# Kernel optimization log

Hardware: AMD Instinct MI355X
Metric: run time of the kernel (lower is better)

The kernel has to match this reference:

```python
import jax, jax.numpy as jnp
import numpy as np

N_EMBED = 2048
N_HEAD = 16
N_GROUP = 4
D_HEAD = N_EMBED // N_HEAD  # 128
GROUP_SIZE = N_HEAD // N_GROUP  # 4
SLIDING_WINDOW = 512
ATTENTION_SINK = 4
POS = 0
ROPE_BASE = 10000.0


def _rope(x, pos):
    # x: (B, T, H, d) -> rotate-half RoPE applied along last dim
    B, T, H, d = x.shape
    half = d // 2
    inv_freq = 1.0 / (ROPE_BASE ** (jnp.arange(half, dtype=jnp.float32) * 2.0 / d))
    t = jnp.arange(T, dtype=jnp.float32) + pos
    ang = t[:, None] * inv_freq[None, :]           # (T, half)
    cos = jnp.cos(ang)[None, :, None, :].astype(x.dtype)
    sin = jnp.sin(ang)[None, :, None, :].astype(x.dtype)
    x1, x2 = x[..., :half], x[..., half:]
    return jnp.concatenate([x1 * cos - x2 * sin, x1 * sin + x2 * cos], axis=-1)


def _sliding_mask(q_len, kv_len):
    i = jnp.arange(q_len)[:, None]
    j = jnp.arange(kv_len)[None, :]
    causal = i >= j
    sink = j < ATTENTION_SINK
    local = j >= i - SLIDING_WINDOW
    return causal & (local | sink)  # (q_len, kv_len) bool


def setup_inputs() -> dict:
    key = jax.random.key(0)
    ks = jax.random.split(key, 9)
    s_in = 1.0 / np.sqrt(N_EMBED)
    x = jax.random.normal(ks[0], (2, 2048, N_EMBED), dtype=jnp.float32)
    # Linear weights stored as (in, out): y = x @ W + b
    Wq = jax.random.uniform(ks[1], (N_EMBED, N_HEAD * D_HEAD), jnp.float32, -s_in, s_in)
    bq = jax.random.uniform(ks[2], (N_HEAD * D_HEAD,), jnp.float32, -s_in, s_in)
    Wk = jax.random.uniform(ks[3], (N_EMBED, N_GROUP * D_HEAD), jnp.float32, -s_in, s_in)
    bk = jax.random.uniform(ks[4], (N_GROUP * D_HEAD,), jnp.float32, -s_in, s_in)
    Wv = jax.random.uniform(ks[5], (N_EMBED, N_GROUP * D_HEAD), jnp.float32, -s_in, s_in)
    bv = jax.random.uniform(ks[6], (N_GROUP * D_HEAD,), jnp.float32, -s_in, s_in)
    Wo = jax.random.uniform(ks[7], (N_EMBED, N_EMBED), jnp.float32, -s_in, s_in)
    bo = jax.random.uniform(ks[8], (N_EMBED,), jnp.float32, -s_in, s_in)
    return {"x": x, "Wq": Wq, "bq": bq, "Wk": Wk, "bk": bk,
            "Wv": Wv, "bv": bv, "Wo": Wo, "bo": bo}


def reference(x, Wq, bq, Wk, bk, Wv, bv, Wo, bo):
    B, T, C = x.shape
    scale = D_HEAD ** -0.5
    Q = (x @ Wq + bq).reshape(B, T, N_HEAD, D_HEAD)
    K = (x @ Wk + bk).reshape(B, T, N_GROUP, D_HEAD)
    V = (x @ Wv + bv).reshape(B, T, N_GROUP, D_HEAD)
    Q = _rope(Q, POS)
    K = _rope(K, POS)
    # (B, G, group, T, d) -- native GQA broadcast instead of repeat_interleave
    Q = Q.transpose(0, 2, 1, 3).reshape(B, N_GROUP, GROUP_SIZE, T, D_HEAD)
    K = K.transpose(0, 2, 1, 3)  # (B, G, T, d)
    V = V.transpose(0, 2, 1, 3)
    scores = jnp.einsum('bghtd,bgsd->bghts', Q, K) * scale  # (B,G,h,T,S)
    mask = _sliding_mask(T, T)[None, None, None, :, :]
    neg = jnp.finfo(scores.dtype).min
    scores = jnp.where(mask, scores, neg)
    W = jax.nn.softmax(scores, axis=-1)
    out = jnp.einsum('bghts,bgsd->bghtd', W, V)  # (B,G,h,T,d)
    out = out.reshape(B, N_HEAD, T, D_HEAD).transpose(0, 2, 1, 3).reshape(B, T, C)
    return out @ Wo + bo
```

## Files before the change

### kernel.cpp

```cpp
#include <hip/hip_runtime.h>
#include <hip/hip_bf16.h>
#include <cstdint>
#include <cstddef>


typedef short s16;
typedef short short8 __attribute__((ext_vector_type(8)));
typedef short s16x4  __attribute__((ext_vector_type(4)));
typedef float f32x4  __attribute__((ext_vector_type(4)));

#define MFMA16(a, b, c) __builtin_amdgcn_mfma_f32_16x16x32_bf16((a), (b), (c), 0, 0, 0)

__device__ __forceinline__ float bf2f(s16 u) {
    union { float f; uint32_t i; } v;
    v.i = ((uint32_t)(uint16_t)u) << 16;
    return v.f;
}
__device__ __forceinline__ s16 f2bf(float f) {
    union { float f; uint32_t i; } v;
    v.f = f;
    uint32_t r = v.i + 0x7FFFu + ((v.i >> 16) & 1u);
    return (s16)(r >> 16);
}

__device__ __forceinline__ void gload16(const s16* g, s16* l) {
    __builtin_amdgcn_global_load_lds(
        (const __attribute__((address_space(1))) void*)g,
        (__attribute__((address_space(3))) void*)l, 16, 0, 0);
}

__global__ __launch_bounds__(256)
void cast_bf16(const float* __restrict__ in, s16* __restrict__ out)
{
    size_t i = ((size_t)blockIdx.x * 256 + threadIdx.x) * 8;
    f32x4 f0 = *(const f32x4*)(in + i);
    f32x4 f1 = *(const f32x4*)(in + i + 4);
    short8 h;
    h[0]=f2bf(f0[0]); h[1]=f2bf(f0[1]); h[2]=f2bf(f0[2]); h[3]=f2bf(f0[3]);
    h[4]=f2bf(f1[0]); h[5]=f2bf(f1[1]); h[6]=f2bf(f1[2]); h[7]=f2bf(f1[3]);
    *(short8*)(out + i) = h;
}

__global__ __launch_bounds__(256)
void castT3(const float* __restrict__ Wq, const float* __restrict__ Wk,
            const float* __restrict__ Wv, s16* __restrict__ out)
{
    int z = blockIdx.z;
    const float* in; s16* dst; int N;
    if (z == 0)      { in = Wq; dst = out;                        N = 2048; }
    else if (z == 1) { in = Wk; dst = out + (size_t)2048 * 2048;  N = 512; }
    else             { in = Wv; dst = out + (size_t)2560 * 2048;  N = 512; }
    int n0 = blockIdx.x * 32, k0 = blockIdx.y * 32;
    if (n0 >= N) return;

    __shared__ float t[32][33];
    int tx = threadIdx.x & 31, ty = threadIdx.x >> 5;
    for (int i = 0; i < 32; i += 8)
        t[ty + i][tx] = in[(size_t)(k0 + ty + i) * N + n0 + tx];
    __syncthreads();
    for (int i = 0; i < 32; i += 8)
        dst[(size_t)(n0 + ty + i) * 2048 + k0 + tx] = f2bf(t[tx][ty + i]);
}

__global__ __launch_bounds__(256)
void castT(const float* __restrict__ in, s16* __restrict__ out)
{
    __shared__ float t[32][33];
    int n0 = blockIdx.x * 32, k0 = blockIdx.y * 32;
    int tx = threadIdx.x & 31, ty = threadIdx.x >> 5;
    for (int i = 0; i < 32; i += 8)
        t[ty + i][tx] = in[(size_t)(k0 + ty + i) * 2048 + n0 + tx];
    __syncthreads();
    for (int i = 0; i < 32; i += 8)
        out[(size_t)(n0 + ty + i) * 2048 + k0 + tx] = f2bf(t[tx][ty + i]);
}

template <int MODE>
__global__ __launch_bounds__(256)
void gemm_lds(const s16* __restrict__ A, const s16* __restrict__ Bt,
              const float* __restrict__ b0, const float* __restrict__ b1,
              const float* __restrict__ b2,
              void* __restrict__ o0, void* __restrict__ o1, void* __restrict__ o2,
              int M, int N, int K)
{
    __shared__ s16 As[128 * 32];
    __shared__ s16 Bs[128 * 32];

    const int tid  = threadIdx.x;
    const int m0   = blockIdx.x * 128, n0 = blockIdx.y * 128;
    const int lane = tid & 63, wv = tid >> 6;
    const int wm   = (wv >> 1) * 64, wn = (wv & 1) * 64;
    const int fr   = lane & 15, fq = lane >> 4;

    const int srow = wv * 16 + (lane >> 2);
    const int koff = (lane & 3) * 8;
    const s16* ga0 = A  + (size_t)(m0 + srow) * K + koff;
    const s16* ga1 = A  + (size_t)(m0 + 64 + srow) * K + koff;
    const s16* gb0 = Bt + (size_t)(n0 + srow) * K + koff;
    const s16* gb1 = Bt + (size_t)(n0 + 64 + srow) * K + koff;
    s16* la0 = &As[(wv * 16) * 32];
    s16* la1 = &As[(64 + wv * 16) * 32];
    s16* lb0 = &Bs[(wv * 16) * 32];
    s16* lb1 = &Bs[(64 + wv * 16) * 32];

    const s16* pa[4];
    const s16* pb[4];
    #pragma unroll
    for (int i = 0; i < 4; i++) {
        pa[i] = &As[(wm + i * 16 + fr) * 32 + fq * 8];
        pb[i] = &Bs[(wn + i * 16 + fr) * 32 + fq * 8];
    }

    f32x4 acc[4][4] = {};

    for (int k0 = 0; k0 < K; k0 += 32) {
        __syncthreads();
        gload16(ga0 + k0, la0);
        gload16(ga1 + k0, la1);
        gload16(gb0 + k0, lb0);
        gload16(gb1 + k0, lb1);
        __syncthreads();

        short8 af[4], bfr[4];
        #pragma unroll
        for (int i = 0; i < 4; i++) af[i] = *(const short8*)pa[i];
        #pragma unroll
        for (int i = 0; i < 4; i++) bfr[i] = *(const short8*)pb[i];

        #pragma unroll
        for (int mi = 0; mi < 4; mi++)
            #pragma unroll
            for (int ni = 0; ni < 4; ni++)
                acc[mi][ni] = MFMA16(af[mi], bfr[ni], acc[mi][ni]);
    }

    #pragma unroll
    for (int mi = 0; mi < 4; mi++)
        #pragma unroll
        for (int ni = 0; ni < 4; ni++)
            #pragma unroll
            for (int r = 0; r < 4; r++) {
                int m = m0 + wm + mi * 16 + fq * 4 + r;
                int n = n0 + wn + ni * 16 + fr;
                float v = acc[mi][ni][r];
                if (MODE == 0) {
                    if (n < 2048)
                        ((s16*)o0)[(size_t)m * 2048 + n] = f2bf(v + b0[n]);
                    else if (n < 2560)
                        ((s16*)o1)[(size_t)m * 512 + (n - 2048)] = f2bf(v + b1[n - 2048]);
                    else
                        ((s16*)o2)[(size_t)(n - 2560) * 4096 + m] = f2bf(v + b2[n - 2560]);
                } else {
                    ((float*)o0)[(size_t)m * N + n] = v + b0[n];
                }
            }
}

__global__ __launch_bounds__(256)
void rope2_kernel(s16* __restrict__ Qb, s16* __restrict__ Kb)
{
    int bx = blockIdx.x;
    s16* buf; int nheads; int idx;
    if (bx < 16384) { buf = Qb; nheads = 16; idx = bx * 256 + threadIdx.x; }
    else            { buf = Kb; nheads = 4;  idx = (bx - 16384) * 256 + threadIdx.x; }

    int i   = idx & 63;
    int hi  = idx >> 6;
    int h   = hi % nheads;
    int row = hi / nheads;
    int t   = row & 2047;

    float inv_freq = __powf(10000.0f, -(float)i * (1.0f / 64.0f));
    float ang = (float)t * inv_freq;
    float c = cosf(ang);
    float s = sinf(ang);

    size_t base = (size_t)row * ((size_t)nheads * 128) + (size_t)h * 128 + i;
    float x1 = bf2f(buf[base]);
    float x2 = bf2f(buf[base + 64]);
    buf[base]      = f2bf(x1 * c - x2 * s);
    buf[base + 64] = f2bf(x1 * s + x2 * c);
}

__global__ __launch_bounds__(256)
void attn_kernel(const s16* __restrict__ Q, const s16* __restrict__ Kb,
                 const s16* __restrict__ Vt, s16* __restrict__ At)
{
    __shared__ s16 Ks[2][32][136];
    __shared__ s16 Vs[2][128][40];
    __shared__ s16 Ps[4][16][40];

    const int b = blockIdx.z;
    const int h = blockIdx.y, g = h >> 2;
    const int t0 = (31 - blockIdx.x) * 64;
    const int tid = threadIdx.x, lane = tid & 63, wv = tid >> 6;
    const int fr = lane & 15, fq = lane >> 4;
    const int tw = t0 + wv * 16;
    s16* O = At + (size_t)b * 4194304;

    const float SCL2 = 0.12751743f;
    const float NEG  = -1e9f;
    const float THR2 = 11.541560f;

    int kr[2], kc[2], vd[2], vc[2];
    const s16 *gK[2], *gV[2];
    #pragma unroll
    for (int it = 0; it < 2; it++) {
        int idx = it * 2048 + tid * 8;
        kr[it] = idx >> 7;  kc[it] = idx & 127;
        vd[it] = idx >> 5;  vc[it] = idx & 31;
        gK[it] = Kb + (size_t)(b * 2048 + kr[it]) * 512 + g * 128 + kc[it];
        gV[it] = Vt + (size_t)(g * 128 + vd[it]) * 4096 + b * 2048 + vc[it];
    }

    short8 qf[4];
    {
        const s16* qrow = Q + (size_t)(b * 2048 + tw + fr) * 2048 + h * 128 + fq * 8;
        qf[0] = *(const short8*)(qrow);
        qf[1] = *(const short8*)(qrow + 32);
        qf[2] = *(const short8*)(qrow + 64);
        qf[3] = *(const short8*)(qrow + 96);
    }

    f32x4 Oacc[8] = {};
    float m2 = NEG, l_s = 0.0f;
    const int tq = tw + fr;

    int lo = t0 - 512; if (lo < 0) lo = 0;
    const int c0   = lo >> 5;
    const int cend = (t0 + 63) >> 5;
    const int nch  = cend - c0 + 1 + (c0 > 0 ? 1 : 0);

    #define CHUNKBASE(ic) ((((c0) > 0) ? ((ic) == 0 ? 0 : c0 + (ic) - 1) : (ic)) * 32)

    short8 kpre[2], vpre[2];
    {
        int kb = CHUNKBASE(0);
        #pragma unroll
        for (int it = 0; it < 2; it++) {
            kpre[it] = *(const short8*)(gK[it] + (size_t)kb * 512);
            vpre[it] = *(const short8*)(gV[it] + kb);
        }
        #pragma unroll
        for (int it = 0; it < 2; it++) {
            *(short8*)&Ks[0][kr[it]][kc[it]] = kpre[it];
            *(short8*)&Vs[0][vd[it]][vc[it]] = vpre[it];
        }
    }
    __syncthreads();

    for (int ic = 0; ic < nch; ic++) {
        const int cur = ic & 1;
        const int kbase = CHUNKBASE(ic);
        const bool pre = (ic + 1 < nch);
        if (pre) {
            int kb = CHUNKBASE(ic + 1);
            #pragma unroll
            for (int it = 0; it < 2; it++) {
                kpre[it] = *(const short8*)(gK[it] + (size_t)kb * 512);
                vpre[it] = *(const short8*)(gV[it] + kb);
            }
        }

        f32x4 sc[2] = {{0.f,0.f,0.f,0.f},{0.f,0.f,0.f,0.f}};
        __builtin_amdgcn_s_setprio(1);
        #pragma unroll
        for (int kn = 0; kn < 2; kn++)
            #pragma unroll
            for (int dc = 0; dc < 4; dc++) {
                short8 kf = *(const short8*)&Ks[cur][kn * 16 + fr][dc * 32 + fq * 8];
                sc[kn] = MFMA16(kf, qf[dc], sc[kn]);
            }
        __builtin_amdgcn_s_setprio(0);

        float sv[8];
        #pragma unroll
        for (int kn = 0; kn < 2; kn++)
            #pragma unroll
            for (int r = 0; r < 4; r++) {
                int j = kbase + kn * 16 + fq * 4 + r;
                bool ok = (j <= tq) && ((j >= tq - 512) || (j < 4));
                sv[kn * 4 + r] = ok ? sc[kn][r] * SCL2 : NEG;
            }

        float cm = fmaxf(sv[0], sv[1]);
        #pragma unroll
        for (int i = 2; i < 8; i++) cm = fmaxf(cm, sv[i]);
        cm = fmaxf(cm, __shfl_xor(cm, 16));
        cm = fmaxf(cm, __shfl_xor(cm, 32));

        if (__any(cm > m2 + THR2)) {
            float nm    = fmaxf(m2, cm);
            float alpha = exp2f(m2 - nm);
            m2  = nm;
            l_s *= alpha;
            #pragma unroll
            for (int r = 0; r < 4; r++) {
                float ar = __shfl(alpha, (lane & 48) + fq * 4 + r);
                #pragma unroll
                for (int n0 = 0; n0 < 8; n0++) Oacc[n0][r] *= ar;
            }
        }

        float p[8], ps = 0.0f;
        #pragma unroll
        for (int i = 0; i < 8; i++) { p[i] = exp2f(sv[i] - m2); ps += p[i]; }
        ps += __shfl_xor(ps, 16);
        ps += __shfl_xor(ps, 32);
        l_s += ps;

        s16x4 w0, w1;
        #pragma unroll
        for (int r = 0; r < 4; r++) { w0[r] = f2bf(p[r]); w1[r] = f2bf(p[4 + r]); }
        *(s16x4*)&Ps[wv][fr][fq * 4]      = w0;
        *(s16x4*)&Ps[wv][fr][16 + fq * 4] = w1;
        __threadfence_block();
        short8 pf = *(const short8*)&Ps[wv][fr][fq * 8];

        __builtin_amdgcn_s_setprio(1);
        #pragma unroll
        for (int n0 = 0; n0 < 8; n0++) {
            short8 vf = *(const short8*)&Vs[cur][n0 * 16 + fr][fq * 8];
            Oacc[n0] = MFMA16(pf, vf, Oacc[n0]);
        }
        __builtin_amdgcn_s_setprio(0);

        if (pre) {
            #pragma unroll
            for (int it = 0; it < 2; it++) {
                *(short8*)&Ks[cur ^ 1][kr[it]][kc[it]] = kpre[it];
                *(short8*)&Vs[cur ^ 1][vd[it]][vc[it]] = vpre[it];
            }
            __syncthreads();
        }
    }

    float linv[4];
    #pragma unroll
    for (int r = 0; r < 4; r++)
        linv[r] = 1.0f / __shfl(l_s, (lane & 48) + fq * 4 + r);
    #pragma unroll
    for (int n0 = 0; n0 < 8; n0++)
        #pragma unroll
        for (int r = 0; r < 4; r++) {
            int t = tw + fq * 4 + r;
            O[(size_t)t * 2048 + h * 128 + n0 * 16 + fr] =
                f2bf(Oacc[n0][r] * linv[r]);
        }
}

extern "C" void kernel_launch(void* const* d_in, const int* in_sizes, int n_in,
                              void* d_out, int out_size, void* d_ws, size_t ws_size,
                              hipStream_t stream)
{
    const float* x  = (const float*)d_in[0];
    const float* Wq = (const float*)d_in[1];
    const float* bq = (const float*)d_in[2];
    const float* Wk = (const float*)d_in[3];
    const float* bk = (const float*)d_in[4];
    const float* Wv = (const float*)d_in[5];
    const float* bv = (const float*)d_in[6];
    const float* Wo = (const float*)d_in[7];
    const float* bo = (const float*)d_in[8];
    float* out = (float*)d_out;

    if (ws_size < 33554432) return;

    char* ws = (char*)d_ws;
    s16* xb    = (s16*)(ws + 0);
    s16* At    = (s16*)(ws + 0);
    s16* Wqkvt = (s16*)(ws + 16777216);
    s16* Wot   = (s16*)(ws + 16777216);
    s16* Qb    = (s16*)d_out;
    s16* Kb    = (s16*)((char*)d_out + 16777216);
    s16* Vt    = (s16*)((char*)d_out + 20971520);

    cast_bf16<<<4096, 256, 0, stream>>>(x, xb);

    castT3<<<dim3(64, 64, 3), 256, 0, stream>>>(Wq, Wk, Wv, Wqkvt);

    gemm_lds<0><<<dim3(32, 24), 256, 0, stream>>>(xb, Wqkvt, bq, bk, bv,
                                                  Qb, Kb, Vt, 4096, 3072, 2048);

    rope2_kernel<<<20480, 256, 0, stream>>>(Qb, Kb);

    castT<<<dim3(64, 64), 256, 0, stream>>>(Wo, Wot);

    attn_kernel<<<dim3(32, 16, 2), 256, 0, stream>>>(Qb, Kb, Vt, At);

    gemm_lds<2><<<dim3(32, 16), 256, 0, stream>>>(At, Wot, bo, nullptr, nullptr,
                                                  out, nullptr, nullptr,
                                                  4096, 2048, 2048);
}
```

Before: 347.1 us.

## Replace 128x128 GEMM with double-buffered swizzled 256x256 tile GEMM

Both projection GEMMs now use a 256x256 block tile with 8 waves, K-step 64, XOR-swizzled LDS layout, and double-buffered shared memory. Global loads for the next K tile are issued in quarters interleaved with the MFMA phases, with explicit waitcnt/barrier scheduling and setprio. This aims to raise arithmetic intensity, cut LDS bank conflicts and hide global latency. Grids shrink to 192 and 128 blocks, which may underfill the 256 CUs, and 128 KB of LDS per block limits occupancy.

Result: slower. 493.3 us (+42.1%).

```diff
diff --git a/kernel.cpp b/kernel.cpp
--- a/kernel.cpp
+++ b/kernel.cpp
@@ -76,66 +76,109 @@
 }
 
 template <int MODE>
-__global__ __launch_bounds__(256)
-void gemm_lds(const s16* __restrict__ A, const s16* __restrict__ Bt,
-              const float* __restrict__ b0, const float* __restrict__ b1,
-              const float* __restrict__ b2,
-              void* __restrict__ o0, void* __restrict__ o1, void* __restrict__ o2,
-              int M, int N, int K)
-{
-    __shared__ s16 As[128 * 32];
-    __shared__ s16 Bs[128 * 32];
+__global__ __launch_bounds__(512, 2)
+void gemm256(const s16* __restrict__ A, const s16* __restrict__ Bt,
+             const float* __restrict__ b0, const float* __restrict__ b1,
+             const float* __restrict__ b2,
+             void* __restrict__ o0, void* __restrict__ o1, void* __restrict__ o2,
+             int M, int N, int K)
+{
+    __shared__ s16 As[2][16384];
+    __shared__ s16 Bs[2][16384];
 
     const int tid  = threadIdx.x;
-    const int m0   = blockIdx.x * 128, n0 = blockIdx.y * 128;
     const int lane = tid & 63, wv = tid >> 6;
-    const int wm   = (wv >> 1) * 64, wn = (wv & 1) * 64;
-    const int fr   = lane & 15, fq = lane >> 4;
-
-    const int srow = wv * 16 + (lane >> 2);
-    const int koff = (lane & 3) * 8;
-    const s16* ga0 = A  + (size_t)(m0 + srow) * K + koff;
-    const s16* ga1 = A  + (size_t)(m0 + 64 + srow) * K + koff;
-    const s16* gb0 = Bt + (size_t)(n0 + srow) * K + koff;
-    const s16* gb1 = Bt + (size_t)(n0 + 64 + srow) * K + koff;
-    s16* la0 = &As[(wv * 16) * 32];
-    s16* la1 = &As[(64 + wv * 16) * 32];
-    s16* lb0 = &Bs[(wv * 16) * 32];
-    s16* lb1 = &Bs[(64 + wv * 16) * 32];
-
-    const s16* pa[4];
-    const s16* pb[4];
-    #pragma unroll
-    for (int i = 0; i < 4; i++) {
-        pa[i] = &As[(wm + i * 16 + fr) * 32 + fq * 8];
-        pb[i] = &Bs[(wn + i * 16 + fr) * 32 + fq * 8];
-    }
-
-    f32x4 acc[4][4] = {};
-
-    for (int k0 = 0; k0 < K; k0 += 32) {
-        __syncthreads();
-        gload16(ga0 + k0, la0);
-        gload16(ga1 + k0, la1);
-        gload16(gb0 + k0, lb0);
-        gload16(gb1 + k0, lb1);
-        __syncthreads();
-
-        short8 af[4], bfr[4];
-        #pragma unroll
-        for (int i = 0; i < 4; i++) af[i] = *(const short8*)pa[i];
-        #pragma unroll
-        for (int i = 0; i < 4; i++) bfr[i] = *(const short8*)pb[i];
-
-        #pragma unroll
-        for (int mi = 0; mi < 4; mi++)
-            #pragma unroll
-            for (int ni = 0; ni < 4; ni++)
-                acc[mi][ni] = MFMA16(af[mi], bfr[ni], acc[mi][ni]);
-    }
-
-    #pragma unroll
-    for (int mi = 0; mi < 4; mi++)
+    const int m0 = blockIdx.x * 256, n0 = blockIdx.y * 256;
+    const int wm = (wv >> 2) * 128;
+    const int wn = (wv & 3) * 64;
+    const int fr = lane & 15, fq = lane >> 4;
+    const int hA = wm >> 7;
+    const int hB = wn >> 7;
+    const int NT = K >> 6;
+
+    const int rs = wv * 8 + (lane >> 3);
+    const int cg = ((lane & 7) ^ (rs & 7)) << 3;
+    const s16* gs[2][2][2];
+    #pragma unroll
+    for (int hh = 0; hh < 2; hh++) {
+        gs[0][hh][0] = A  + (size_t)(m0 + hh * 128 + rs)      * K + cg;
+        gs[0][hh][1] = A  + (size_t)(m0 + hh * 128 + rs + 64) * K + cg;
+        gs[1][hh][0] = Bt + (size_t)(n0 + hh * 128 + rs)      * K + cg;
+        gs[1][hh][1] = Bt + (size_t)(n0 + hh * 128 + rs + 64) * K + cg;
+    }
+
+    const int kx0 = (fq ^ (fr & 7)) << 4;
+    const int kx1 = kx0 ^ 64;
+    const char* aBase[2] = {
+        (const char*)&As[0][0] + hA * 16384 + fr * 128,
+        (const char*)&As[1][0] + hA * 16384 + fr * 128 };
+    const char* bBase[2] = {
+        (const char*)&Bs[0][0] + hB * 16384 + ((wn & 64) + fr) * 128,
+        (const char*)&Bs[1][0] + hB * 16384 + ((wn & 64) + fr) * 128 };
+
+    f32x4 acc[8][4] = {};
+
+    #pragma unroll
+    for (int u = 0; u < 4; u++) {
+        const int op = u >> 1, hh = u & 1;
+        s16* d = (op ? &Bs[0][0] : &As[0][0]) + hh * 8192 + wv * 512;
+        gload16(gs[op][hh][0], d);
+        gload16(gs[op][hh][1], d + 4096);
+    }
+    asm volatile("s_waitcnt vmcnt(0)");
+    __builtin_amdgcn_sched_barrier(0);
+    __builtin_amdgcn_s_barrier();
+
+    short8 bf[4][2];
+    for (int t = 0; t < NT; t++) {
+        const int rb = t & 1, wb = rb ^ 1;
+        const bool pre = (t + 1 < NT);
+        #pragma unroll
+        for (int q = 0; q < 4; q++) {
+            short8 af[2][2];
+            #pragma unroll
+            for (int m2 = 0; m2 < 2; m2++)
+                #pragma unroll
+                for (int k2 = 0; k2 < 2; k2++)
+                    af[m2][k2] = *(const short8*)(aBase[rb] + (2 * q + m2) * 2048
+                                                  + (k2 ? kx1 : kx0));
+            if (q == 0) {
+                #pragma unroll
+                for (int ni = 0; ni < 4; ni++)
+                    #pragma unroll
+                    for (int k2 = 0; k2 < 2; k2++)
+                        bf[ni][k2] = *(const short8*)(bBase[rb] + ni * 2048
+                                                      + (k2 ? kx1 : kx0));
+            }
+            if (pre) {
+                const int op = q >> 1, hh = q & 1;
+                s16* d = (op ? &Bs[wb][0] : &As[wb][0]) + hh * 8192 + wv * 512;
+                gload16(gs[op][hh][0] + (t + 1) * 64, d);
+                gload16(gs[op][hh][1] + (t + 1) * 64, d + 4096);
+            }
+            __builtin_amdgcn_s_barrier();
+            asm volatile("s_waitcnt lgkmcnt(0)");
+            __builtin_amdgcn_sched_barrier(0);
+            __builtin_amdgcn_s_setprio(1);
+            #pragma unroll
+            for (int m2 = 0; m2 < 2; m2++)
+                #pragma unroll
+                for (int ni = 0; ni < 4; ni++)
+                    #pragma unroll
+                    for (int k2 = 0; k2 < 2; k2++)
+                        acc[2 * q + m2][ni] =
+                            MFMA16(af[m2][k2], bf[ni][k2], acc[2 * q + m2][ni]);
+            __builtin_amdgcn_s_setprio(0);
+            if (q == 3) {
+                asm volatile("s_waitcnt vmcnt(0)");
+                __builtin_amdgcn_sched_barrier(0);
+            }
+            __builtin_amdgcn_s_barrier();
+        }
+    }
+
+    #pragma unroll
+    for (int mi = 0; mi < 8; mi++)
         #pragma unroll
         for (int ni = 0; ni < 4; ni++)
             #pragma unroll
@@ -379,8 +422,8 @@
 
     castT3<<<dim3(64, 64, 3), 256, 0, stream>>>(Wq, Wk, Wv, Wqkvt);
 
-    gemm_lds<0><<<dim3(32, 24), 256, 0, stream>>>(xb, Wqkvt, bq, bk, bv,
-                                                  Qb, Kb, Vt, 4096, 3072, 2048);
+    gemm256<0><<<dim3(16, 12), 512, 0, stream>>>(xb, Wqkvt, bq, bk, bv,
+                                                 Qb, Kb, Vt, 4096, 3072, 2048);
 
     rope2_kernel<<<20480, 256, 0, stream>>>(Qb, Kb);
 
@@ -388,7 +431,7 @@
 
     attn_kernel<<<dim3(32, 16, 2), 256, 0, stream>>>(Qb, Kb, Vt, At);
 
-    gemm_lds<2><<<dim3(32, 16), 256, 0, stream>>>(At, Wot, bo, nullptr, nullptr,
-                                                  out, nullptr, nullptr,
-                                                  4096, 2048, 2048);
-}
+    gemm256<2><<<dim3(16, 8), 512, 0, stream>>>(At, Wot, bo, nullptr, nullptr,
+                                                out, nullptr, nullptr,
+                                                4096, 2048, 2048);
+}
```

## Pipeline GEMM global-to-LDS loads through a four-slot ring with swizzled LDS

Applied to the files above, without the earlier changes.

Replaces the single-buffered GEMM mainloop with a four-slot LDS ring that prefetches two K-tiles ahead. Waits use vmcnt so only one barrier is needed per iteration instead of two, and global load latency overlaps with MFMA work. It also XOR-swizzles the LDS column layout to cut bank conflicts on fragment reads, raises wave priority around the MFMA block, and sets launch bounds for two blocks per CU. In exchange, LDS use grows to 64 KB per block, which can limit occupancy, and the hand-written waitcnt logic depends on gload16 issuing exactly one VMEM op per call.

Result: slower. 374.1 us (+7.8%).

```diff
diff --git a/kernel.cpp b/kernel.cpp
--- a/kernel.cpp
+++ b/kernel.cpp
@@ -76,63 +76,81 @@
 }
 
 template <int MODE>
-__global__ __launch_bounds__(256)
-void gemm_lds(const s16* __restrict__ A, const s16* __restrict__ Bt,
-              const float* __restrict__ b0, const float* __restrict__ b1,
-              const float* __restrict__ b2,
-              void* __restrict__ o0, void* __restrict__ o1, void* __restrict__ o2,
-              int M, int N, int K)
-{
-    __shared__ s16 As[128 * 32];
-    __shared__ s16 Bs[128 * 32];
+__global__ __launch_bounds__(256, 2)
+void gemm_ring(const s16* __restrict__ A, const s16* __restrict__ Bt,
+               const float* __restrict__ b0, const float* __restrict__ b1,
+               const float* __restrict__ b2,
+               void* __restrict__ o0, void* __restrict__ o1, void* __restrict__ o2,
+               int M, int N, int K)
+{
+    __shared__ s16 As[4][4096];
+    __shared__ s16 Bs[4][4096];
 
     const int tid  = threadIdx.x;
-    const int m0   = blockIdx.x * 128, n0 = blockIdx.y * 128;
     const int lane = tid & 63, wv = tid >> 6;
-    const int wm   = (wv >> 1) * 64, wn = (wv & 1) * 64;
-    const int fr   = lane & 15, fq = lane >> 4;
-
-    const int srow = wv * 16 + (lane >> 2);
-    const int koff = (lane & 3) * 8;
-    const s16* ga0 = A  + (size_t)(m0 + srow) * K + koff;
-    const s16* ga1 = A  + (size_t)(m0 + 64 + srow) * K + koff;
-    const s16* gb0 = Bt + (size_t)(n0 + srow) * K + koff;
-    const s16* gb1 = Bt + (size_t)(n0 + 64 + srow) * K + koff;
-    s16* la0 = &As[(wv * 16) * 32];
-    s16* la1 = &As[(64 + wv * 16) * 32];
-    s16* lb0 = &Bs[(wv * 16) * 32];
-    s16* lb1 = &Bs[(64 + wv * 16) * 32];
-
-    const s16* pa[4];
-    const s16* pb[4];
-    #pragma unroll
-    for (int i = 0; i < 4; i++) {
-        pa[i] = &As[(wm + i * 16 + fr) * 32 + fq * 8];
-        pb[i] = &Bs[(wn + i * 16 + fr) * 32 + fq * 8];
-    }
+    const int m0 = blockIdx.x * 128, n0 = blockIdx.y * 128;
+    const int wm = (wv >> 1) * 64, wn = (wv & 1) * 64;
+    const int fr = lane & 15, fq = lane >> 4;
+    const int NT = K >> 5;
+
+    const int rsub = tid >> 2;
+    const int cg = (((tid & 3) ^ ((tid >> 2) & 3) ^ ((tid >> 4) & 3))) << 3;
+    const s16* gA0 = A  + (size_t)(m0 + rsub) * K + cg;
+    const s16* gA1 = A  + (size_t)(m0 + 64 + rsub) * K + cg;
+    const s16* gB0 = Bt + (size_t)(n0 + rsub) * K + cg;
+    const s16* gB1 = Bt + (size_t)(n0 + 64 + rsub) * K + cg;
+
+    const int kxr = ((fq ^ (fr & 3) ^ ((fr >> 2) & 3)) << 4);
+    const char* aRow = (const char*)As + (wm + fr) * 64 + kxr;
+    const char* bRow = (const char*)Bs + (wn + fr) * 64 + kxr;
 
     f32x4 acc[4][4] = {};
 
-    for (int k0 = 0; k0 < K; k0 += 32) {
-        __syncthreads();
-        gload16(ga0 + k0, la0);
-        gload16(ga1 + k0, la1);
-        gload16(gb0 + k0, lb0);
-        gload16(gb1 + k0, lb1);
-        __syncthreads();
+#define STAGE(tt) do { const int _bi = (tt) & 3;                             \
+        s16* _da = &As[_bi][0] + wv * 512;                                   \
+        s16* _db = &Bs[_bi][0] + wv * 512;                                   \
+        gload16(gA0 + (tt) * 32, _da);                                       \
+        gload16(gA1 + (tt) * 32, _da + 2048);                                \
+        gload16(gB0 + (tt) * 32, _db);                                       \
+        gload16(gB1 + (tt) * 32, _db + 2048); } while (0)
+
+    STAGE(0);
+    STAGE(1);
+    asm volatile("s_waitcnt vmcnt(4)");
+    __builtin_amdgcn_sched_barrier(0);
+    __builtin_amdgcn_s_barrier();
+
+    for (int t = 0; t < NT; t++) {
+        const int rb = t & 3;
+        if (t + 2 < NT) STAGE(t + 2);
 
         short8 af[4], bfr[4];
-        #pragma unroll
-        for (int i = 0; i < 4; i++) af[i] = *(const short8*)pa[i];
-        #pragma unroll
-        for (int i = 0; i < 4; i++) bfr[i] = *(const short8*)pb[i];
-
+        const char* aP = aRow + rb * 8192;
+        const char* bP = bRow + rb * 8192;
+        #pragma unroll
+        for (int i = 0; i < 4; i++) af[i]  = *(const short8*)(aP + i * 1024);
+        #pragma unroll
+        for (int i = 0; i < 4; i++) bfr[i] = *(const short8*)(bP + i * 1024);
+
+        asm volatile("s_waitcnt lgkmcnt(0)");
+        __builtin_amdgcn_sched_barrier(0);
+        __builtin_amdgcn_s_setprio(1);
         #pragma unroll
         for (int mi = 0; mi < 4; mi++)
             #pragma unroll
             for (int ni = 0; ni < 4; ni++)
                 acc[mi][ni] = MFMA16(af[mi], bfr[ni], acc[mi][ni]);
+        __builtin_amdgcn_s_setprio(0);
+
+        if (t + 1 < NT) {
+            __builtin_amdgcn_sched_barrier(0);
+            if (t + 2 < NT) asm volatile("s_waitcnt vmcnt(4)");
+            else            asm volatile("s_waitcnt vmcnt(0)");
+            __builtin_amdgcn_sched_barrier(0);
+            __builtin_amdgcn_s_barrier();
+        }
     }
+#undef STAGE
 
     #pragma unroll
     for (int mi = 0; mi < 4; mi++)
@@ -379,8 +397,8 @@
 
     castT3<<<dim3(64, 64, 3), 256, 0, stream>>>(Wq, Wk, Wv, Wqkvt);
 
-    gemm_lds<0><<<dim3(32, 24), 256, 0, stream>>>(xb, Wqkvt, bq, bk, bv,
-                                                  Qb, Kb, Vt, 4096, 3072, 2048);
+    gemm_ring<0><<<dim3(32, 24), 256, 0, stream>>>(xb, Wqkvt, bq, bk, bv,
+                                                   Qb, Kb, Vt, 4096, 3072, 2048);
 
     rope2_kernel<<<20480, 256, 0, stream>>>(Qb, Kb);
 
@@ -388,7 +406,7 @@
 
     attn_kernel<<<dim3(32, 16, 2), 256, 0, stream>>>(Qb, Kb, Vt, At);
 
-    gemm_lds<2><<<dim3(32, 16), 256, 0, stream>>>(At, Wot, bo, nullptr, nullptr,
-                                                  out, nullptr, nullptr,
-                                                  4096, 2048, 2048);
-}
+    gemm_ring<2><<<dim3(32, 16), 256, 0, stream>>>(At, Wot, bo, nullptr, nullptr,
+                                                   out, nullptr, nullptr,
+                                                   4096, 2048, 2048);
+}
```

## Double GEMM K-tile to 64 with XOR-swizzled LDS layout

Applied to the files above, without the earlier changes.

Both projection GEMMs now load a 128x64 K-slab per iteration instead of 128x32, halving the number of barrier pairs per K loop and doubling MFMA work per sync. The LDS tile is stored with an XOR swizzle on 16-byte chunks so that the fragment reads avoid bank conflicts. Wave priority is raised around the MFMA block, and launch bounds request 3 blocks per CU. In exchange LDS use per block doubles to 32 KB, and the swizzle indexing must match between the global-to-LDS writes and the fragment reads.

Result: faster. 311.4 us (-10.3%).

```diff
diff --git a/kernel.cpp b/kernel.cpp
--- a/kernel.cpp
+++ b/kernel.cpp
@@ -76,62 +76,71 @@
 }
 
 template <int MODE>
-__global__ __launch_bounds__(256)
-void gemm_lds(const s16* __restrict__ A, const s16* __restrict__ Bt,
-              const float* __restrict__ b0, const float* __restrict__ b1,
-              const float* __restrict__ b2,
-              void* __restrict__ o0, void* __restrict__ o1, void* __restrict__ o2,
-              int M, int N, int K)
-{
-    __shared__ s16 As[128 * 32];
-    __shared__ s16 Bs[128 * 32];
+__global__ __launch_bounds__(256, 3)
+void gemm_bk64(const s16* __restrict__ A, const s16* __restrict__ Bt,
+               const float* __restrict__ b0, const float* __restrict__ b1,
+               const float* __restrict__ b2,
+               void* __restrict__ o0, void* __restrict__ o1, void* __restrict__ o2,
+               int M, int N, int K)
+{
+    __shared__ s16 As[128 * 64];
+    __shared__ s16 Bs[128 * 64];
 
     const int tid  = threadIdx.x;
-    const int m0   = blockIdx.x * 128, n0 = blockIdx.y * 128;
     const int lane = tid & 63, wv = tid >> 6;
-    const int wm   = (wv >> 1) * 64, wn = (wv & 1) * 64;
-    const int fr   = lane & 15, fq = lane >> 4;
-
-    const int srow = wv * 16 + (lane >> 2);
-    const int koff = (lane & 3) * 8;
-    const s16* ga0 = A  + (size_t)(m0 + srow) * K + koff;
-    const s16* ga1 = A  + (size_t)(m0 + 64 + srow) * K + koff;
-    const s16* gb0 = Bt + (size_t)(n0 + srow) * K + koff;
-    const s16* gb1 = Bt + (size_t)(n0 + 64 + srow) * K + koff;
-    s16* la0 = &As[(wv * 16) * 32];
-    s16* la1 = &As[(64 + wv * 16) * 32];
-    s16* lb0 = &Bs[(wv * 16) * 32];
-    s16* lb1 = &Bs[(64 + wv * 16) * 32];
-
-    const s16* pa[4];
-    const s16* pb[4];
+    const int m0 = blockIdx.x * 128, n0 = blockIdx.y * 128;
+    const int wm = (wv >> 1) * 64, wn = (wv & 1) * 64;
+    const int fr = lane & 15, fq = lane >> 4;
+    const int NT = K >> 6;
+
+    const int srow = tid >> 3;
+    const int scol = ((tid & 7) ^ (srow & 7)) << 3;
+    const s16* gA[4];
+    const s16* gB[4];
     #pragma unroll
-    for (int i = 0; i < 4; i++) {
-        pa[i] = &As[(wm + i * 16 + fr) * 32 + fq * 8];
-        pb[i] = &Bs[(wn + i * 16 + fr) * 32 + fq * 8];
-    }
+    for (int s = 0; s < 4; s++) {
+        gA[s] = A  + (size_t)(m0 + s * 32 + srow) * K + scol;
+        gB[s] = Bt + (size_t)(n0 + s * 32 + srow) * K + scol;
+    }
+
+    const int kc0 = (fq ^ (fr & 7)) << 4;
+    const int kc1 = kc0 ^ 64;
+    const char* aRow = (const char*)As + (wm + fr) * 128;
+    const char* bRow = (const char*)Bs + (wn + fr) * 128;
 
     f32x4 acc[4][4] = {};
 
-    for (int k0 = 0; k0 < K; k0 += 32) {
+    for (int t = 0; t < NT; t++) {
         __syncthreads();
-        gload16(ga0 + k0, la0);
-        gload16(ga1 + k0, la1);
-        gload16(gb0 + k0, lb0);
-        gload16(gb1 + k0, lb1);
+        #pragma unroll
+        for (int s = 0; s < 4; s++)
+            gload16(gA[s] + t * 64, As + s * 2048 + wv * 512);
+        #pragma unroll
+        for (int s = 0; s < 4; s++)
+            gload16(gB[s] + t * 64, Bs + s * 2048 + wv * 512);
         __syncthreads();
 
-        short8 af[4], bfr[4];
-        #pragma unroll
-        for (int i = 0; i < 4; i++) af[i] = *(const short8*)pa[i];
-        #pragma unroll
-        for (int i = 0; i < 4; i++) bfr[i] = *(const short8*)pb[i];
-
+        short8 af[4][2], bfr[4][2];
+        #pragma unroll
+        for (int mi = 0; mi < 4; mi++) {
+            af[mi][0] = *(const short8*)(aRow + mi * 2048 + kc0);
+            af[mi][1] = *(const short8*)(aRow + mi * 2048 + kc1);
+        }
+        #pragma unroll
+        for (int ni = 0; ni < 4; ni++) {
+            bfr[ni][0] = *(const short8*)(bRow + ni * 2048 + kc0);
+            bfr[ni][1] = *(const short8*)(bRow + ni * 2048 + kc1);
+        }
+
+        __builtin_amdgcn_s_setprio(1);
         #pragma unroll
         for (int mi = 0; mi < 4; mi++)
             #pragma unroll
-            for (int ni = 0; ni < 4; ni++)
-                acc[mi][ni] = MFMA16(af[mi], bfr[ni], acc[mi][ni]);
+            for (int ni = 0; ni < 4; ni++) {
+                acc[mi][ni] = MFMA16(af[mi][0], bfr[ni][0], acc[mi][ni]);
+                acc[mi][ni] = MFMA16(af[mi][1], bfr[ni][1], acc[mi][ni]);
+            }
+        __builtin_amdgcn_s_setprio(0);
     }
 
     #pragma unroll
@@ -379,8 +388,8 @@
 
     castT3<<<dim3(64, 64, 3), 256, 0, stream>>>(Wq, Wk, Wv, Wqkvt);
 
-    gemm_lds<0><<<dim3(32, 24), 256, 0, stream>>>(xb, Wqkvt, bq, bk, bv,
-                                                  Qb, Kb, Vt, 4096, 3072, 2048);
+    gemm_bk64<0><<<dim3(32, 24), 256, 0, stream>>>(xb, Wqkvt, bq, bk, bv,
+                                                   Qb, Kb, Vt, 4096, 3072, 2048);
 
     rope2_kernel<<<20480, 256, 0, stream>>>(Qb, Kb);
 
@@ -388,7 +397,7 @@
 
     attn_kernel<<<dim3(32, 16, 2), 256, 0, stream>>>(Qb, Kb, Vt, At);
 
-    gemm_lds<2><<<dim3(32, 16), 256, 0, stream>>>(At, Wot, bo, nullptr, nullptr,
-                                                  out, nullptr, nullptr,
-                                                  4096, 2048, 2048);
-}
+    gemm_bk64<2><<<dim3(32, 16), 256, 0, stream>>>(At, Wot, bo, nullptr, nullptr,
+                                                   out, nullptr, nullptr,
+                                                   4096, 2048, 2048);
+}
```
